# Optimization experiments

Measured on AMD Instinct MI355X. Metric: run time of the kernel, lower is better.

Reference implementation:

```python
import jax, jax.numpy as jnp
import numpy as np

N = 50000
F_IN = 256
H1, D1 = 8, 8            # conv1: 8 heads x 8 dims, concat -> 64
H2, C = 8, 16            # conv2: 8 heads x num_classes, concat -> 128
NEG_SLOPE = 0.2


def setup_inputs() -> dict:
    key = jax.random.key(0)
    ks = jax.random.split(key, 10)
    x = jax.random.normal(ks[0], (N, F_IN), dtype=jnp.float32)
    edge_index = jax.random.randint(ks[1], (2, 800000), 0, N, dtype=jnp.int64)
    s1 = 1.0 / np.sqrt(F_IN)
    s2 = 1.0 / np.sqrt(H1 * D1)
    return {
        "x": x,
        "edge_index": edge_index,
        "W1": jax.random.normal(ks[2], (F_IN, H1 * D1), dtype=jnp.float32) * s1,
        "a1_src": jax.random.normal(ks[3], (H1, D1), dtype=jnp.float32) * s2,
        "a1_dst": jax.random.normal(ks[4], (H1, D1), dtype=jnp.float32) * s2,
        "b1": jnp.zeros((H1 * D1,), dtype=jnp.float32),
        "W2": jax.random.normal(ks[5], (H1 * D1, H2 * C), dtype=jnp.float32) * s2,
        "a2_src": jax.random.normal(ks[6], (H2, C), dtype=jnp.float32) * (1.0 / np.sqrt(C)),
        "a2_dst": jax.random.normal(ks[7], (H2, C), dtype=jnp.float32) * (1.0 / np.sqrt(C)),
        "b2": jnp.zeros((H2 * C,), dtype=jnp.float32),
    }


def _add_self_loops(edge_index, n):
    loops = jnp.arange(n, dtype=edge_index.dtype)
    return jnp.concatenate([edge_index, jnp.stack([loops, loops])], axis=1)


def _gat_conv(x, src, dst, W, a_src, a_dst, b, heads, out_dim, n):
    # xw: [N, H, O]
    xw = (x @ W).reshape(n, heads, out_dim)
    al_src = jnp.einsum("nho,ho->nh", xw, a_src)  # [N, H]
    al_dst = jnp.einsum("nho,ho->nh", xw, a_dst)
    e = jax.nn.leaky_relu(al_src[src] + al_dst[dst], NEG_SLOPE)  # [E, H]
    # segment softmax over edges sharing a destination node
    e_max = jax.ops.segment_max(e, dst, num_segments=n)
    e_exp = jnp.exp(e - e_max[dst])
    denom = jax.ops.segment_sum(e_exp, dst, num_segments=n)
    alpha = e_exp / (denom[dst] + 1e-16)                          # [E, H]
    msg = xw[src] * alpha[:, :, None]                              # [E, H, O]
    out = jax.ops.segment_sum(msg, dst, num_segments=n)           # [N, H, O]
    return out.reshape(n, heads * out_dim) + b, alpha


def reference(x, edge_index, W1, a1_src, a1_dst, b1, W2, a2_src, a2_dst, b2):
    ei = _add_self_loops(edge_index, N)
    src, dst = ei[0], ei[1]
    # dropout is a no-op at inference (training=False)
    h1, alpha1 = _gat_conv(x, src, dst, W1, a1_src, a1_dst, b1, H1, D1, N)
    h1 = jax.nn.elu(h1)
    h2, _ = _gat_conv(h1, src, dst, W2, a2_src, a2_dst, b2, H2, C, N)
    logp = jax.nn.log_softmax(h2, axis=1)
    return logp, alpha1
```

## Files before the change

### kernel.cpp

```cpp
#include <hip/hip_runtime.h>

#define N_NODES 50000
#define N_EDGES 800000
#define N_TOT   850000
#define NEG 0.2f
#define ELLW 64

#define G1_TILES 391
#define G2_TILES 782

#define NBIN   250
#define NPBIN  200
#define BKBLK  200
#define EPBK   4000
#define BCAP   40
#define OCAP   4096
#define NELLB  250

__device__ __forceinline__ float leaky(float x) { return x > 0.f ? x : NEG * x; }

__device__ __forceinline__ unsigned bf16pk(float a, float b) {
  unsigned ua = __float_as_uint(a), ub = __float_as_uint(b);
  ua = (ua + 0x7FFFu + ((ua >> 16) & 1u)) >> 16;
  ub = (ub + 0x7FFFu + ((ub >> 16) & 1u)) >> 16;
  return ua | (ub << 16);
}
__device__ __forceinline__ float blo(unsigned u) { return __uint_as_float(u << 16); }
__device__ __forceinline__ float bhi(unsigned u) { return __uint_as_float(u & 0xFFFF0000u); }
__device__ __forceinline__ float bh2f(unsigned short h) { return __uint_as_float(((unsigned)h) << 16); }

__global__ __launch_bounds__(256) void bin_k(const int* __restrict__ srcA,
    const int* __restrict__ dstA, unsigned* __restrict__ slots,
    unsigned short* __restrict__ bcnt2, unsigned* __restrict__ ofl, int* __restrict__ ofc)
{
  __shared__ unsigned buf[NBIN][BCAP];
  __shared__ int bc[NBIN];
  const int t = threadIdx.x;
  for (int k = t; k < NBIN; k += 256) bc[k] = 0;
  __syncthreads();
  const int e0 = blockIdx.x * EPBK;
#pragma unroll
  for (int j = 0; j < 4; ++j) {
    int i4 = j * 256 + t;
    if (i4 < EPBK / 4) {
      int4 s4 = ((const int4*)(srcA + e0))[i4];
      int4 d4 = ((const int4*)(dstA + e0))[i4];
      int dd[4] = {d4.x, d4.y, d4.z, d4.w};
      int ss[4] = {s4.x, s4.y, s4.z, s4.w};
#pragma unroll
      for (int q = 0; q < 4; ++q) {
        int bin = dd[q] / NPBIN;
        unsigned rec = (unsigned)dd[q] | ((unsigned)ss[q] << 16);
        int p = atomicAdd(&bc[bin], 1);
        if (p < BCAP) buf[bin][p] = rec;
        else { int g = atomicAdd(ofc, 1); if (g < OCAP) ofl[g] = rec; }
      }
    }
  }
  __syncthreads();
  if (t < NBIN) {
    int c = bc[t]; if (c > BCAP) c = BCAP;
    bcnt2[(size_t)t * BKBLK + blockIdx.x] = (unsigned short)c;
    unsigned* dp = slots + ((size_t)t * BKBLK + blockIdx.x) * BCAP;
    for (int j = 0; j < c; ++j) dp[j] = buf[t][j];
  }
}

__global__ __launch_bounds__(256) void gemm1_ell_k(const float* __restrict__ x,
    const float* __restrict__ W1, const float* __restrict__ a1sv, const float* __restrict__ a1dv,
    unsigned short* __restrict__ xw1h, float* __restrict__ al1s, float* __restrict__ a1dd,
    const unsigned* __restrict__ slots, const unsigned short* __restrict__ bcnt2,
    const unsigned* __restrict__ ofl, const int* __restrict__ ofc,
    int* __restrict__ cnt, unsigned short* __restrict__ ell)
{
  __shared__ __align__(16) char smem[26432];
  const int t = threadIdx.x;
  if (blockIdx.x < NELLB) {
    unsigned short* ell_lds = (unsigned short*)smem;
    int* cnt_lds = (int*)(smem + 25600);
    const int b = blockIdx.x;
    for (int k = t; k < NPBIN; k += 256) cnt_lds[k] = 0;
    __syncthreads();
    if (t < BKBLK) {
      int c = bcnt2[(size_t)b * BKBLK + t];
      const unsigned* sp = slots + ((size_t)b * BKBLK + t) * BCAP;
      for (int j = 0; j < c; ++j) {
        unsigned rec = sp[j];
        int row = (int)(rec & 0xFFFFu) - b * NPBIN;
        int p = atomicAdd(&cnt_lds[row], 1);
        if (p < ELLW) ell_lds[row * ELLW + p] = (unsigned short)(rec >> 16);
      }
    }
    __syncthreads();
    int oc = *ofc; if (oc > OCAP) oc = OCAP;
    for (int i = t; i < oc; i += 256) {
      unsigned rec = ofl[i];
      int d = rec & 0xFFFFu;
      if (d >= b * NPBIN && d < (b + 1) * NPBIN) {
        int p = atomicAdd(&cnt_lds[d - b * NPBIN], 1);
        if (p < ELLW) ell_lds[(d - b * NPBIN) * ELLW + p] = (unsigned short)(rec >> 16);
      }
    }
    __syncthreads();
    const uint4* s4 = (const uint4*)ell_lds;
    uint4* d4 = (uint4*)(ell + (size_t)b * NPBIN * ELLW);
    for (int i = t; i < NPBIN * ELLW / 8; i += 256) d4[i] = s4[i];
    for (int k = t; k < NPBIN; k += 256) cnt[b * NPBIN + k] = cnt_lds[k];
    return;
  }
  float* xs  = (float*)smem;
  float* wsm = (float*)(smem + 16384);
  const int tx = t & 15, ty = t >> 4;
  const int n0 = (blockIdx.x - NELLB) * 128;
  const int nl = t >> 1;
  const int ks = (t & 1) * 16;
  const int wk = t >> 3;
  const int wc = (t & 7) * 8;
  int gn = n0 + nl; if (gn >= N_NODES) gn = N_NODES - 1;
  const float* xrowb = x + (size_t)gn * 256 + ks;

  float acc[8][4];
#pragma unroll
  for (int r = 0; r < 8; ++r)
#pragma unroll
    for (int i = 0; i < 4; ++i) acc[r][i] = 0.f;

  for (int kc = 0; kc < 8; ++kc) {
    const int kb = kc * 32;
    const float4* xp = (const float4*)(xrowb + kb);
    float4 v0 = xp[0], v1 = xp[1], v2 = xp[2], v3 = xp[3];
    const float* wrow = W1 + (size_t)(kb + wk) * 64 + wc;
    float4 w0 = ((const float4*)wrow)[0];
    float4 w1 = ((const float4*)wrow)[1];
    __syncthreads();
    xs[(ks + 0) * 128 + nl] = v0.x;  xs[(ks + 1) * 128 + nl] = v0.y;
    xs[(ks + 2) * 128 + nl] = v0.z;  xs[(ks + 3) * 128 + nl] = v0.w;
    xs[(ks + 4) * 128 + nl] = v1.x;  xs[(ks + 5) * 128 + nl] = v1.y;
    xs[(ks + 6) * 128 + nl] = v1.z;  xs[(ks + 7) * 128 + nl] = v1.w;
    xs[(ks + 8) * 128 + nl] = v2.x;  xs[(ks + 9) * 128 + nl] = v2.y;
    xs[(ks + 10) * 128 + nl] = v2.z; xs[(ks + 11) * 128 + nl] = v2.w;
    xs[(ks + 12) * 128 + nl] = v3.x; xs[(ks + 13) * 128 + nl] = v3.y;
    xs[(ks + 14) * 128 + nl] = v3.z; xs[(ks + 15) * 128 + nl] = v3.w;
    ((float4*)&wsm[wk * 64 + wc])[0] = w0;
    ((float4*)&wsm[wk * 64 + wc])[1] = w1;
    __syncthreads();
#pragma unroll 4
    for (int k = 0; k < 32; ++k) {
      float4 xa = *(const float4*)&xs[k * 128 + ty * 8];
      float4 xb = *(const float4*)&xs[k * 128 + ty * 8 + 4];
      float4 wv = *(const float4*)&wsm[k * 64 + tx * 4];
      float xn[8]; *(float4*)&xn[0] = xa; *(float4*)&xn[4] = xb;
      float wn[4]; *(float4*)wn = wv;
#pragma unroll
      for (int r = 0; r < 8; ++r)
#pragma unroll
        for (int i = 0; i < 4; ++i) acc[r][i] += xn[r] * wn[i];
    }
  }
  float cs[4], cd[4];
#pragma unroll
  for (int i = 0; i < 4; ++i) { cs[i] = a1sv[tx * 4 + i]; cd[i] = a1dv[tx * 4 + i]; }
#pragma unroll
  for (int r = 0; r < 8; ++r) {
    int n = n0 + ty * 8 + r;
    if (n >= N_NODES) break;
    uint2 pk;
    pk.x = bf16pk(acc[r][0], acc[r][1]);
    pk.y = bf16pk(acc[r][2], acc[r][3]);
    *(uint2*)(xw1h + (size_t)n * 64 + tx * 4) = pk;
    float ps = acc[r][0] * cs[0] + acc[r][1] * cs[1] + acc[r][2] * cs[2] + acc[r][3] * cs[3];
    float pd = acc[r][0] * cd[0] + acc[r][1] * cd[1] + acc[r][2] * cd[2] + acc[r][3] * cd[3];
    ps += __shfl_xor(ps, 1);
    pd += __shfl_xor(pd, 1);
    if ((tx & 1) == 0) {
      al1s[n * 8 + (tx >> 1)] = ps;
      a1dd[n * 16 + (tx >> 1)] = pd;
    }
  }
}

__global__ __launch_bounds__(256) void agg1_k(const unsigned short* __restrict__ xw1h,
    const float* __restrict__ al1s, float* __restrict__ a1dd,
    const int* __restrict__ cnt, const unsigned short* __restrict__ ell,
    const float* __restrict__ b1, float* __restrict__ h1)
{
  const int lane = threadIdx.x & 63;
  const int n = blockIdx.x * 4 + (threadIdx.x >> 6);
  if (n >= N_NODES) return;
  const int h = lane >> 3;
  const float ad = a1dd[n * 16 + h];
  float ws = __expf(leaky(al1s[n * 8 + h] + ad));
  float den0 = ws, den1r = 0.f;
  float acc0 = ws * bh2f(xw1h[(size_t)n * 64 + lane]), acc1 = 0.f;
  int num = cnt[n]; if (num > ELLW) num = ELLW;
  const uint4* cp = (const uint4*)(ell + (size_t)n * ELLW);
  int i = 0;
  for (; i + 8 <= num; i += 8) {
    uint4 A = cp[i >> 3];
    int s0 = A.x & 0xFFFF, s1 = (int)(A.x >> 16);
    int s2 = A.y & 0xFFFF, s3 = (int)(A.y >> 16);
    int s4 = A.z & 0xFFFF, s5 = (int)(A.z >> 16);
    int s6 = A.w & 0xFFFF, s7 = (int)(A.w >> 16);
    float l0 = al1s[s0 * 8 + h] + ad, l1 = al1s[s1 * 8 + h] + ad;
    float l2 = al1s[s2 * 8 + h] + ad, l3 = al1s[s3 * 8 + h] + ad;
    float l4 = al1s[s4 * 8 + h] + ad, l5 = al1s[s5 * 8 + h] + ad;
    float l6 = al1s[s6 * 8 + h] + ad, l7 = al1s[s7 * 8 + h] + ad;
    float v0 = bh2f(xw1h[(size_t)s0 * 64 + lane]), v1 = bh2f(xw1h[(size_t)s1 * 64 + lane]);
    float v2 = bh2f(xw1h[(size_t)s2 * 64 + lane]), v3 = bh2f(xw1h[(size_t)s3 * 64 + lane]);
    float v4 = bh2f(xw1h[(size_t)s4 * 64 + lane]), v5 = bh2f(xw1h[(size_t)s5 * 64 + lane]);
    float v6 = bh2f(xw1h[(size_t)s6 * 64 + lane]), v7 = bh2f(xw1h[(size_t)s7 * 64 + lane]);
    float w0 = __expf(leaky(l0)), w1 = __expf(leaky(l1));
    float w2 = __expf(leaky(l2)), w3 = __expf(leaky(l3));
    float w4 = __expf(leaky(l4)), w5 = __expf(leaky(l5));
    float w6 = __expf(leaky(l6)), w7 = __expf(leaky(l7));
    acc0 += w0 * v0; acc1 += w1 * v1; acc0 += w2 * v2; acc1 += w3 * v3;
    acc0 += w4 * v4; acc1 += w5 * v5; acc0 += w6 * v6; acc1 += w7 * v7;
    den0 += w0 + w2 + w4 + w6; den1r += w1 + w3 + w5 + w7;
  }
  for (; i + 4 <= num; i += 4) {
    uint2 A = *(const uint2*)(ell + (size_t)n * ELLW + i);
    int s0 = A.x & 0xFFFF, s1 = (int)(A.x >> 16);
    int s2 = A.y & 0xFFFF, s3 = (int)(A.y >> 16);
    float l0 = al1s[s0 * 8 + h] + ad, l1 = al1s[s1 * 8 + h] + ad;
    float l2 = al1s[s2 * 8 + h] + ad, l3 = al1s[s3 * 8 + h] + ad;
    float v0 = bh2f(xw1h[(size_t)s0 * 64 + lane]), v1 = bh2f(xw1h[(size_t)s1 * 64 + lane]);
    float v2 = bh2f(xw1h[(size_t)s2 * 64 + lane]), v3 = bh2f(xw1h[(size_t)s3 * 64 + lane]);
    float w0 = __expf(leaky(l0)), w1 = __expf(leaky(l1));
    float w2 = __expf(leaky(l2)), w3 = __expf(leaky(l3));
    acc0 += w0 * v0; acc1 += w1 * v1; acc0 += w2 * v2; acc1 += w3 * v3;
    den0 += w0 + w2; den1r += w1 + w3;
  }
  for (; i < num; ++i) {
    int s = ell[(size_t)n * ELLW + i];
    float w = __expf(leaky(al1s[s * 8 + h] + ad));
    acc0 += w * bh2f(xw1h[(size_t)s * 64 + lane]);
    den0 += w;
  }
  float den = den0 + den1r, acc = acc0 + acc1;
  if ((lane & 7) == 0) a1dd[n * 16 + 8 + h] = den;
  float o = acc / (den + 1e-16f) + b1[lane];
  h1[(size_t)n * 64 + lane] = o > 0.f ? o : (__expf(o) - 1.f);
}

__global__ __launch_bounds__(256) void gemm2_alpha_k(const float* __restrict__ h1,
    const float* __restrict__ W2, const float* __restrict__ a2sv, const float* __restrict__ a2dv,
    unsigned* __restrict__ xw2b, float* __restrict__ al2s, float* __restrict__ al2d,
    const int* __restrict__ srcA, const int* __restrict__ dstA,
    const float* __restrict__ al1s, const float* __restrict__ a1dd,
    float* __restrict__ alpha_out)
{
  __shared__ float xs[64 * 64];
  __shared__ float wsm[64 * 128];
  if (blockIdx.x >= G2_TILES) {
    int e = (blockIdx.x - G2_TILES) * 256 + threadIdx.x;
    if (e >= N_TOT) return;
    int s, d;
    if (e < N_EDGES) { s = srcA[e]; d = dstA[e]; }
    else             { s = d = e - N_EDGES; }
    float4 as0 = ((const float4*)(al1s + s * 8))[0];
    float4 as1 = ((const float4*)(al1s + s * 8))[1];
    const float4* dd = (const float4*)(a1dd + d * 16);
    float4 ad0 = dd[0];
    float4 ad1 = dd[1];
    float4 dn0 = dd[2];
    float4 dn1 = dd[3];
    float4 o0, o1;
    o0.x = __expf(leaky(as0.x + ad0.x)) / (dn0.x + 1e-16f);
    o0.y = __expf(leaky(as0.y + ad0.y)) / (dn0.y + 1e-16f);
    o0.z = __expf(leaky(as0.z + ad0.z)) / (dn0.z + 1e-16f);
    o0.w = __expf(leaky(as0.w + ad0.w)) / (dn0.w + 1e-16f);
    o1.x = __expf(leaky(as1.x + ad1.x)) / (dn1.x + 1e-16f);
    o1.y = __expf(leaky(as1.y + ad1.y)) / (dn1.y + 1e-16f);
    o1.z = __expf(leaky(as1.z + ad1.z)) / (dn1.z + 1e-16f);
    o1.w = __expf(leaky(as1.w + ad1.w)) / (dn1.w + 1e-16f);
    ((float4*)(alpha_out + (size_t)e * 8))[0] = o0;
    ((float4*)(alpha_out + (size_t)e * 8))[1] = o1;
    return;
  }
  const int t = threadIdx.x;
  const int tx = t & 15, ty = t >> 4;
  const int n0 = blockIdx.x * 64;
  {
    const int nl = t >> 2;
    const int ks = (t & 3) * 16;
    int gn = n0 + nl; if (gn >= N_NODES) gn = N_NODES - 1;
    const float4* hp = (const float4*)(h1 + (size_t)gn * 64 + ks);
#pragma unroll
    for (int j = 0; j < 4; ++j) {
      float4 v = hp[j];
      xs[(ks + 4 * j + 0) * 64 + nl] = v.x;
      xs[(ks + 4 * j + 1) * 64 + nl] = v.y;
      xs[(ks + 4 * j + 2) * 64 + nl] = v.z;
      xs[(ks + 4 * j + 3) * 64 + nl] = v.w;
    }
    const int wk = t >> 2;
    const int wc = (t & 3) * 32;
    const float4* wp = (const float4*)(W2 + (size_t)wk * 128 + wc);
    float4* wd = (float4*)&wsm[wk * 128 + wc];
#pragma unroll
    for (int j = 0; j < 8; ++j) wd[j] = wp[j];
  }
  __syncthreads();
  float acc[4][8];
#pragma unroll
  for (int r = 0; r < 4; ++r)
#pragma unroll
    for (int i = 0; i < 8; ++i) acc[r][i] = 0.f;
#pragma unroll 4
  for (int k = 0; k < 64; ++k) {
    float4 xa = *(const float4*)&xs[k * 64 + ty * 4];
    float4 wa = *(const float4*)&wsm[k * 128 + tx * 8];
    float4 wb = *(const float4*)&wsm[k * 128 + tx * 8 + 4];
    float xn[4]; *(float4*)xn = xa;
    float wn[8]; *(float4*)&wn[0] = wa; *(float4*)&wn[4] = wb;
#pragma unroll
    for (int r = 0; r < 4; ++r)
#pragma unroll
      for (int i = 0; i < 8; ++i) acc[r][i] += xn[r] * wn[i];
  }
  float cs[8], cd[8];
#pragma unroll
  for (int i = 0; i < 8; ++i) { cs[i] = a2sv[tx * 8 + i]; cd[i] = a2dv[tx * 8 + i]; }
#pragma unroll
  for (int r = 0; r < 4; ++r) {
    int n = n0 + ty * 4 + r;
    if (n >= N_NODES) break;
    uint4 pk;
    pk.x = bf16pk(acc[r][0], acc[r][1]);
    pk.y = bf16pk(acc[r][2], acc[r][3]);
    pk.z = bf16pk(acc[r][4], acc[r][5]);
    pk.w = bf16pk(acc[r][6], acc[r][7]);
    *(uint4*)(xw2b + (size_t)n * 64 + tx * 4) = pk;
    float ps = 0.f, pd = 0.f;
#pragma unroll
    for (int i = 0; i < 8; ++i) { ps += acc[r][i] * cs[i]; pd += acc[r][i] * cd[i]; }
    ps += __shfl_xor(ps, 1);
    pd += __shfl_xor(pd, 1);
    if ((tx & 1) == 0) {
      al2s[n * 8 + (tx >> 1)] = ps;
      al2d[n * 8 + (tx >> 1)] = pd;
    }
  }
}

__global__ __launch_bounds__(256) void agg2_k(const unsigned* __restrict__ xw2b,
    const float* __restrict__ al2s, const float* __restrict__ al2d,
    const int* __restrict__ cnt, const unsigned short* __restrict__ ell,
    const float* __restrict__ b2, float* __restrict__ logp)
{
  const int lane = threadIdx.x & 63;
  const int n = blockIdx.x * 4 + (threadIdx.x >> 6);
  if (n >= N_NODES) return;
  const int h = lane >> 3;
  const float ad = al2d[n * 8 + h];
  float ws = __expf(leaky(al2s[n * 8 + h] + ad));
  unsigned su = xw2b[(size_t)n * 64 + lane];
  float den0 = ws, den1r = 0.f;
  float ax0 = ws * blo(su), ay0 = ws * bhi(su), ax1 = 0.f, ay1 = 0.f;
  int num = cnt[n]; if (num > ELLW) num = ELLW;
  const uint4* cp = (const uint4*)(ell + (size_t)n * ELLW);
  int i = 0;
  for (; i + 8 <= num; i += 8) {
    uint4 A = cp[i >> 3];
    int s0 = A.x & 0xFFFF, s1 = (int)(A.x >> 16);
    int s2 = A.y & 0xFFFF, s3 = (int)(A.y >> 16);
    int s4 = A.z & 0xFFFF, s5 = (int)(A.z >> 16);
    int s6 = A.w & 0xFFFF, s7 = (int)(A.w >> 16);
    float l0 = al2s[s0 * 8 + h] + ad, l1 = al2s[s1 * 8 + h] + ad;
    float l2 = al2s[s2 * 8 + h] + ad, l3 = al2s[s3 * 8 + h] + ad;
    float l4 = al2s[s4 * 8 + h] + ad, l5 = al2s[s5 * 8 + h] + ad;
    float l6 = al2s[s6 * 8 + h] + ad, l7 = al2s[s7 * 8 + h] + ad;
    unsigned u0 = xw2b[(size_t)s0 * 64 + lane], u1 = xw2b[(size_t)s1 * 64 + lane];
    unsigned u2 = xw2b[(size_t)s2 * 64 + lane], u3 = xw2b[(size_t)s3 * 64 + lane];
    unsigned u4 = xw2b[(size_t)s4 * 64 + lane], u5 = xw2b[(size_t)s5 * 64 + lane];
    unsigned u6 = xw2b[(size_t)s6 * 64 + lane], u7 = xw2b[(size_t)s7 * 64 + lane];
    float w0 = __expf(leaky(l0)), w1 = __expf(leaky(l1));
    float w2 = __expf(leaky(l2)), w3 = __expf(leaky(l3));
    float w4 = __expf(leaky(l4)), w5 = __expf(leaky(l5));
    float w6 = __expf(leaky(l6)), w7 = __expf(leaky(l7));
    ax0 += w0 * blo(u0); ay0 += w0 * bhi(u0);
    ax1 += w1 * blo(u1); ay1 += w1 * bhi(u1);
    ax0 += w2 * blo(u2); ay0 += w2 * bhi(u2);
    ax1 += w3 * blo(u3); ay1 += w3 * bhi(u3);
    ax0 += w4 * blo(u4); ay0 += w4 * bhi(u4);
    ax1 += w5 * blo(u5); ay1 += w5 * bhi(u5);
    ax0 += w6 * blo(u6); ay0 += w6 * bhi(u6);
    ax1 += w7 * blo(u7); ay1 += w7 * bhi(u7);
    den0 += w0 + w2 + w4 + w6; den1r += w1 + w3 + w5 + w7;
  }
  for (; i + 4 <= num; i += 4) {
    uint2 A = *(const uint2*)(ell + (size_t)n * ELLW + i);
    int s0 = A.x & 0xFFFF, s1 = (int)(A.x >> 16);
    int s2 = A.y & 0xFFFF, s3 = (int)(A.y >> 16);
    float l0 = al2s[s0 * 8 + h] + ad, l1 = al2s[s1 * 8 + h] + ad;
    float l2 = al2s[s2 * 8 + h] + ad, l3 = al2s[s3 * 8 + h] + ad;
    unsigned u0 = xw2b[(size_t)s0 * 64 + lane], u1 = xw2b[(size_t)s1 * 64 + lane];
    unsigned u2 = xw2b[(size_t)s2 * 64 + lane], u3 = xw2b[(size_t)s3 * 64 + lane];
    float w0 = __expf(leaky(l0)), w1 = __expf(leaky(l1));
    float w2 = __expf(leaky(l2)), w3 = __expf(leaky(l3));
    ax0 += w0 * blo(u0); ay0 += w0 * bhi(u0);
    ax1 += w1 * blo(u1); ay1 += w1 * bhi(u1);
    ax0 += w2 * blo(u2); ay0 += w2 * bhi(u2);
    ax1 += w3 * blo(u3); ay1 += w3 * bhi(u3);
    den0 += w0 + w2; den1r += w1 + w3;
  }
  for (; i < num; ++i) {
    int s = ell[(size_t)n * ELLW + i];
    float w = __expf(leaky(al2s[s * 8 + h] + ad));
    unsigned u = xw2b[(size_t)s * 64 + lane];
    ax0 += w * blo(u); ay0 += w * bhi(u); den0 += w;
  }
  float inv = 1.f / (den0 + den1r + 1e-16f);
  float o0 = (ax0 + ax1) * inv + b2[2 * lane];
  float o1 = (ay0 + ay1) * inv + b2[2 * lane + 1];
  float mx = fmaxf(o0, o1);
#pragma unroll
  for (int off = 1; off < 64; off <<= 1) mx = fmaxf(mx, __shfl_xor(mx, off));
  float se = __expf(o0 - mx) + __expf(o1 - mx);
#pragma unroll
  for (int off = 1; off < 64; off <<= 1) se += __shfl_xor(se, off);
  float lse = mx + __logf(se);
  float2 o; o.x = o0 - lse; o.y = o1 - lse;
  ((float2*)logp)[(size_t)n * 64 + lane] = o;
}

extern "C" void kernel_launch(void* const* d_in, const int* in_sizes, int n_in,
                              void* d_out, int out_size, void* d_ws, size_t ws_size,
                              hipStream_t stream)
{
  const float* x   = (const float*)d_in[0];
  const int*   ei  = (const int*)d_in[1];
  const float* W1  = (const float*)d_in[2];
  const float* a1s = (const float*)d_in[3];
  const float* a1d = (const float*)d_in[4];
  const float* b1  = (const float*)d_in[5];
  const float* W2  = (const float*)d_in[6];
  const float* a2s = (const float*)d_in[7];
  const float* a2d = (const float*)d_in[8];
  const float* b2  = (const float*)d_in[9];
  const int* srcA = ei;
  const int* dstA = ei + N_EDGES;

  char* ws = (char*)d_ws;
  unsigned short* xw1h = (unsigned short*)ws;            ws += (size_t)N_NODES * 64 * 2;
  float* h1    = (float*)ws;  ws += (size_t)N_NODES * 64 * 4;
  unsigned* xw2b = (unsigned*)ws; ws += (size_t)N_NODES * 64 * 4;
  float* al1s_ = (float*)ws;  ws += (size_t)N_NODES * 8 * 4;
  float* a1dd_ = (float*)ws;  ws += (size_t)N_NODES * 16 * 4;
  float* al2s_ = (float*)ws;  ws += (size_t)N_NODES * 8 * 4;
  float* al2d_ = (float*)ws;  ws += (size_t)N_NODES * 8 * 4;
  int* cnt    = (int*)ws;     ws += (size_t)N_NODES * 4;
  unsigned short* ell = (unsigned short*)ws; ws += (size_t)N_NODES * ELLW * 2;
  unsigned* slots = (unsigned*)ws; ws += (size_t)NBIN * BKBLK * BCAP * 4;
  unsigned short* bcnt2 = (unsigned short*)ws; ws += (size_t)NBIN * BKBLK * 2;
  unsigned* ofl = (unsigned*)ws; ws += (size_t)OCAP * 4;
  int* ofc = (int*)ws; ws += 16;

  float* logp      = (float*)d_out;
  float* alpha_out = logp + (size_t)N_NODES * 128;

  hipMemsetAsync(ofc, 0, sizeof(int), stream);

  bin_k<<<BKBLK, 256, 0, stream>>>(srcA, dstA, slots, bcnt2, ofl, ofc);
  gemm1_ell_k<<<NELLB + G1_TILES, 256, 0, stream>>>(
      x, W1, a1s, a1d, xw1h, al1s_, a1dd_, slots, bcnt2, ofl, ofc, cnt, ell);
  agg1_k<<<(N_NODES + 3) / 4, 256, 0, stream>>>(xw1h, al1s_, a1dd_, cnt, ell, b1, h1);
  gemm2_alpha_k<<<G2_TILES + (N_TOT + 255) / 256, 256, 0, stream>>>(
      h1, W2, a2s, a2d, xw2b, al2s_, al2d_, srcA, dstA, al1s_, a1dd_, alpha_out);
  agg2_k<<<(N_NODES + 3) / 4, 256, 0, stream>>>(xw2b, al2s_, al2d_, cnt, ell, b2, logp);
}
```

Baseline: 160.6 us.

## Fuse edge binning into GEMM1 launch and split ELL build into own kernel

Edge binning moves into the GEMM1 kernel as extra blocks, so binning overlaps with the dense matmul. ELL construction now runs in a separate small kernel between GEMM1 and agg1, reading slots as vectorized uint4 loads into registers. BCAP drops from 40 to 32 to fit the LDS and the vector loads, which pushes more records onto the global overflow list. GEMM1 also prefetches the next k-chunk of x and W1 into registers before the compute loop, and slot writeout is spread across all four wavefronts.

Result: no change. 158.9 us (-1.0%).

```diff
diff --git a/kernel.cpp b/kernel.cpp
--- a/kernel.cpp
+++ b/kernel.cpp
@@ -13,9 +13,8 @@
 #define NPBIN  200
 #define BKBLK  200
 #define EPBK   4000
-#define BCAP   40
+#define BCAP   32
 #define OCAP   4096
-#define NELLB  250
 
 __device__ __forceinline__ float leaky(float x) { return x > 0.f ? x : NEG * x; }
 
@@ -29,89 +28,52 @@
 __device__ __forceinline__ float bhi(unsigned u) { return __uint_as_float(u & 0xFFFF0000u); }
 __device__ __forceinline__ float bh2f(unsigned short h) { return __uint_as_float(((unsigned)h) << 16); }
 
-__global__ __launch_bounds__(256) void bin_k(const int* __restrict__ srcA,
-    const int* __restrict__ dstA, unsigned* __restrict__ slots,
-    unsigned short* __restrict__ bcnt2, unsigned* __restrict__ ofl, int* __restrict__ ofc)
-{
-  __shared__ unsigned buf[NBIN][BCAP];
-  __shared__ int bc[NBIN];
-  const int t = threadIdx.x;
-  for (int k = t; k < NBIN; k += 256) bc[k] = 0;
-  __syncthreads();
-  const int e0 = blockIdx.x * EPBK;
-#pragma unroll
-  for (int j = 0; j < 4; ++j) {
-    int i4 = j * 256 + t;
-    if (i4 < EPBK / 4) {
-      int4 s4 = ((const int4*)(srcA + e0))[i4];
-      int4 d4 = ((const int4*)(dstA + e0))[i4];
-      int dd[4] = {d4.x, d4.y, d4.z, d4.w};
-      int ss[4] = {s4.x, s4.y, s4.z, s4.w};
-#pragma unroll
-      for (int q = 0; q < 4; ++q) {
-        int bin = dd[q] / NPBIN;
-        unsigned rec = (unsigned)dd[q] | ((unsigned)ss[q] << 16);
-        int p = atomicAdd(&bc[bin], 1);
-        if (p < BCAP) buf[bin][p] = rec;
-        else { int g = atomicAdd(ofc, 1); if (g < OCAP) ofl[g] = rec; }
-      }
-    }
-  }
-  __syncthreads();
-  if (t < NBIN) {
-    int c = bc[t]; if (c > BCAP) c = BCAP;
-    bcnt2[(size_t)t * BKBLK + blockIdx.x] = (unsigned short)c;
-    unsigned* dp = slots + ((size_t)t * BKBLK + blockIdx.x) * BCAP;
-    for (int j = 0; j < c; ++j) dp[j] = buf[t][j];
-  }
-}
-
-__global__ __launch_bounds__(256) void gemm1_ell_k(const float* __restrict__ x,
+__global__ __launch_bounds__(256) void bin_gemm1_k(const float* __restrict__ x,
     const float* __restrict__ W1, const float* __restrict__ a1sv, const float* __restrict__ a1dv,
     unsigned short* __restrict__ xw1h, float* __restrict__ al1s, float* __restrict__ a1dd,
-    const unsigned* __restrict__ slots, const unsigned short* __restrict__ bcnt2,
-    const unsigned* __restrict__ ofl, const int* __restrict__ ofc,
-    int* __restrict__ cnt, unsigned short* __restrict__ ell)
-{
-  __shared__ __align__(16) char smem[26432];
+    const int* __restrict__ srcA, const int* __restrict__ dstA,
+    unsigned* __restrict__ slots, unsigned short* __restrict__ bcnt2,
+    unsigned* __restrict__ ofl, int* __restrict__ ofc)
+{
+  __shared__ __align__(16) char smem[33024];
   const int t = threadIdx.x;
-  if (blockIdx.x < NELLB) {
-    unsigned short* ell_lds = (unsigned short*)smem;
-    int* cnt_lds = (int*)(smem + 25600);
-    const int b = blockIdx.x;
-    for (int k = t; k < NPBIN; k += 256) cnt_lds[k] = 0;
+  if (blockIdx.x < BKBLK) {
+    unsigned (*buf)[BCAP] = (unsigned(*)[BCAP])smem;
+    int* bc = (int*)(smem + 32000);
+    for (int k = t; k < NBIN; k += 256) bc[k] = 0;
     __syncthreads();
-    if (t < BKBLK) {
-      int c = bcnt2[(size_t)b * BKBLK + t];
-      const unsigned* sp = slots + ((size_t)b * BKBLK + t) * BCAP;
-      for (int j = 0; j < c; ++j) {
-        unsigned rec = sp[j];
-        int row = (int)(rec & 0xFFFFu) - b * NPBIN;
-        int p = atomicAdd(&cnt_lds[row], 1);
-        if (p < ELLW) ell_lds[row * ELLW + p] = (unsigned short)(rec >> 16);
+    const int e0 = blockIdx.x * EPBK;
+#pragma unroll
+    for (int j = 0; j < 4; ++j) {
+      int i4 = j * 256 + t;
+      if (i4 < EPBK / 4) {
+        int4 s4 = ((const int4*)(srcA + e0))[i4];
+        int4 d4 = ((const int4*)(dstA + e0))[i4];
+        int dd[4] = {d4.x, d4.y, d4.z, d4.w};
+        int ss[4] = {s4.x, s4.y, s4.z, s4.w};
+#pragma unroll
+        for (int q = 0; q < 4; ++q) {
+          int bin = dd[q] / NPBIN;
+          unsigned rec = (unsigned)dd[q] | ((unsigned)ss[q] << 16);
+          int p = atomicAdd(&bc[bin], 1);
+          if (p < BCAP) buf[bin][p] = rec;
+          else { int g = atomicAdd(ofc, 1); if (g < OCAP) ofl[g] = rec; }
+        }
       }
     }
     __syncthreads();
-    int oc = *ofc; if (oc > OCAP) oc = OCAP;
-    for (int i = t; i < oc; i += 256) {
-      unsigned rec = ofl[i];
-      int d = rec & 0xFFFFu;
-      if (d >= b * NPBIN && d < (b + 1) * NPBIN) {
-        int p = atomicAdd(&cnt_lds[d - b * NPBIN], 1);
-        if (p < ELLW) ell_lds[(d - b * NPBIN) * ELLW + p] = (unsigned short)(rec >> 16);
-      }
-    }
-    __syncthreads();
-    const uint4* s4 = (const uint4*)ell_lds;
-    uint4* d4 = (uint4*)(ell + (size_t)b * NPBIN * ELLW);
-    for (int i = t; i < NPBIN * ELLW / 8; i += 256) d4[i] = s4[i];
-    for (int k = t; k < NPBIN; k += 256) cnt[b * NPBIN + k] = cnt_lds[k];
+    const int wv = t >> 6, ln = t & 63;
+    for (int b = wv; b < NBIN; b += 4) {
+      int c = bc[b]; if (c > BCAP) c = BCAP;
+      if (ln == 0) bcnt2[(size_t)b * BKBLK + blockIdx.x] = (unsigned short)c;
+      if (ln < c) slots[((size_t)b * BKBLK + blockIdx.x) * BCAP + ln] = buf[b][ln];
+    }
     return;
   }
   float* xs  = (float*)smem;
   float* wsm = (float*)(smem + 16384);
   const int tx = t & 15, ty = t >> 4;
-  const int n0 = (blockIdx.x - NELLB) * 128;
+  const int n0 = (blockIdx.x - BKBLK) * 128;
   const int nl = t >> 1;
   const int ks = (t & 1) * 16;
   const int wk = t >> 3;
@@ -125,25 +87,35 @@
 #pragma unroll
     for (int i = 0; i < 4; ++i) acc[r][i] = 0.f;
 
+  float4 xv0, xv1, xv2, xv3, wv0, wv1;
+  {
+    const float4* xp = (const float4*)xrowb;
+    xv0 = xp[0]; xv1 = xp[1]; xv2 = xp[2]; xv3 = xp[3];
+    const float* wrow = W1 + (size_t)wk * 64 + wc;
+    wv0 = ((const float4*)wrow)[0];
+    wv1 = ((const float4*)wrow)[1];
+  }
   for (int kc = 0; kc < 8; ++kc) {
-    const int kb = kc * 32;
-    const float4* xp = (const float4*)(xrowb + kb);
-    float4 v0 = xp[0], v1 = xp[1], v2 = xp[2], v3 = xp[3];
-    const float* wrow = W1 + (size_t)(kb + wk) * 64 + wc;
-    float4 w0 = ((const float4*)wrow)[0];
-    float4 w1 = ((const float4*)wrow)[1];
     __syncthreads();
-    xs[(ks + 0) * 128 + nl] = v0.x;  xs[(ks + 1) * 128 + nl] = v0.y;
-    xs[(ks + 2) * 128 + nl] = v0.z;  xs[(ks + 3) * 128 + nl] = v0.w;
-    xs[(ks + 4) * 128 + nl] = v1.x;  xs[(ks + 5) * 128 + nl] = v1.y;
-    xs[(ks + 6) * 128 + nl] = v1.z;  xs[(ks + 7) * 128 + nl] = v1.w;
-    xs[(ks + 8) * 128 + nl] = v2.x;  xs[(ks + 9) * 128 + nl] = v2.y;
-    xs[(ks + 10) * 128 + nl] = v2.z; xs[(ks + 11) * 128 + nl] = v2.w;
-    xs[(ks + 12) * 128 + nl] = v3.x; xs[(ks + 13) * 128 + nl] = v3.y;
-    xs[(ks + 14) * 128 + nl] = v3.z; xs[(ks + 15) * 128 + nl] = v3.w;
-    ((float4*)&wsm[wk * 64 + wc])[0] = w0;
-    ((float4*)&wsm[wk * 64 + wc])[1] = w1;
+    xs[(ks + 0) * 128 + nl] = xv0.x;  xs[(ks + 1) * 128 + nl] = xv0.y;
+    xs[(ks + 2) * 128 + nl] = xv0.z;  xs[(ks + 3) * 128 + nl] = xv0.w;
+    xs[(ks + 4) * 128 + nl] = xv1.x;  xs[(ks + 5) * 128 + nl] = xv1.y;
+    xs[(ks + 6) * 128 + nl] = xv1.z;  xs[(ks + 7) * 128 + nl] = xv1.w;
+    xs[(ks + 8) * 128 + nl] = xv2.x;  xs[(ks + 9) * 128 + nl] = xv2.y;
+    xs[(ks + 10) * 128 + nl] = xv2.z; xs[(ks + 11) * 128 + nl] = xv2.w;
+    xs[(ks + 12) * 128 + nl] = xv3.x; xs[(ks + 13) * 128 + nl] = xv3.y;
+    xs[(ks + 14) * 128 + nl] = xv3.z; xs[(ks + 15) * 128 + nl] = xv3.w;
+    ((float4*)&wsm[wk * 64 + wc])[0] = wv0;
+    ((float4*)&wsm[wk * 64 + wc])[1] = wv1;
     __syncthreads();
+    if (kc < 7) {
+      const int kb = (kc + 1) * 32;
+      const float4* xp = (const float4*)(xrowb + kb);
+      xv0 = xp[0]; xv1 = xp[1]; xv2 = xp[2]; xv3 = xp[3];
+      const float* wrow = W1 + (size_t)(kb + wk) * 64 + wc;
+      wv0 = ((const float4*)wrow)[0];
+      wv1 = ((const float4*)wrow)[1];
+    }
 #pragma unroll 4
     for (int k = 0; k < 32; ++k) {
       float4 xa = *(const float4*)&xs[k * 128 + ty * 8];
@@ -177,6 +149,49 @@
       a1dd[n * 16 + (tx >> 1)] = pd;
     }
   }
+}
+
+__global__ __launch_bounds__(256) void ell_k(const unsigned* __restrict__ slots,
+    const unsigned short* __restrict__ bcnt2, const unsigned* __restrict__ ofl,
+    const int* __restrict__ ofc, int* __restrict__ cnt, unsigned short* __restrict__ ell)
+{
+  __shared__ unsigned short ell_lds[NPBIN * ELLW];
+  __shared__ int cnt_lds[NPBIN];
+  const int t = threadIdx.x;
+  const int b = blockIdx.x;
+  for (int k = t; k < NPBIN; k += 256) cnt_lds[k] = 0;
+  __syncthreads();
+  if (t < BKBLK) {
+    int c = bcnt2[(size_t)b * BKBLK + t];
+    const uint4* sp4 = (const uint4*)(slots + ((size_t)b * BKBLK + t) * BCAP);
+    uint4 R[8];
+#pragma unroll
+    for (int q = 0; q < 8; ++q) R[q] = sp4[q];
+#pragma unroll
+    for (int j = 0; j < BCAP; ++j) {
+      if (j < c) {
+        unsigned rec = ((const unsigned*)R)[j];
+        int row = (int)(rec & 0xFFFFu) - b * NPBIN;
+        int p = atomicAdd(&cnt_lds[row], 1);
+        if (p < ELLW) ell_lds[row * ELLW + p] = (unsigned short)(rec >> 16);
+      }
+    }
+  }
+  __syncthreads();
+  int oc = *ofc; if (oc > OCAP) oc = OCAP;
+  for (int i = t; i < oc; i += 256) {
+    unsigned rec = ofl[i];
+    int d = rec & 0xFFFFu;
+    if (d >= b * NPBIN && d < (b + 1) * NPBIN) {
+      int p = atomicAdd(&cnt_lds[d - b * NPBIN], 1);
+      if (p < ELLW) ell_lds[(d - b * NPBIN) * ELLW + p] = (unsigned short)(rec >> 16);
+    }
+  }
+  __syncthreads();
+  const uint4* s4 = (const uint4*)ell_lds;
+  uint4* d4 = (uint4*)(ell + (size_t)b * NPBIN * ELLW);
+  for (int i = t; i < NPBIN * ELLW / 8; i += 256) d4[i] = s4[i];
+  for (int k = t; k < NPBIN; k += 256) cnt[b * NPBIN + k] = cnt_lds[k];
 }
 
 __global__ __launch_bounds__(256) void agg1_k(const unsigned short* __restrict__ xw1h,
@@ -461,9 +476,9 @@
 
   hipMemsetAsync(ofc, 0, sizeof(int), stream);
 
-  bin_k<<<BKBLK, 256, 0, stream>>>(srcA, dstA, slots, bcnt2, ofl, ofc);
-  gemm1_ell_k<<<NELLB + G1_TILES, 256, 0, stream>>>(
-      x, W1, a1s, a1d, xw1h, al1s_, a1dd_, slots, bcnt2, ofl, ofc, cnt, ell);
+  bin_gemm1_k<<<BKBLK + G1_TILES, 256, 0, stream>>>(
+      x, W1, a1s, a1d, xw1h, al1s_, a1dd_, srcA, dstA, slots, bcnt2, ofl, ofc);
+  ell_k<<<NBIN, 256, 0, stream>>>(slots, bcnt2, ofl, ofc, cnt, ell);
   agg1_k<<<(N_NODES + 3) / 4, 256, 0, stream>>>(xw1h, al1s_, a1dd_, cnt, ell, b1, h1);
   gemm2_alpha_k<<<G2_TILES + (N_TOT + 255) / 256, 256, 0, stream>>>(
       h1, W2, a2s, a2d, xw2b, al2s_, al2d_, srcA, dstA, al1s_, a1dd_, alpha_out);
```
